# Optimization experiments

Measured on AMD Instinct MI355X. Metric: run time of the kernel, lower is better.

Reference implementation:

```python
import jax, jax.numpy as jnp
import numpy as np

B, F, V, E = 16384, 39, 100000, 16
D0, D1, D2 = 32, 32, 32

def setup_inputs() -> dict:
    key = jax.random.key(0)
    ks = jax.random.split(key, 12)
    return {
        "Xi": jax.random.randint(ks[0], (B, F, 1), 0, V),
        "Xv": jax.random.uniform(ks[1], (B, F), dtype=jnp.float32),
        "emb_tables": jax.random.normal(ks[2], (F, V, E), dtype=jnp.float32),
        "w_first": jax.random.normal(ks[3], (D0, F, E), dtype=jnp.float32),
        "w_inner": jax.random.normal(ks[4], (D0, F, E), dtype=jnp.float32),
        "lin1_W": jax.random.normal(ks[5], (D1, D0), dtype=jnp.float32) * 0.1,
        "lin1_b": jax.random.normal(ks[6], (D1,), dtype=jnp.float32) * 0.1,
        "lin2_W": jax.random.normal(ks[7], (D2, D1), dtype=jnp.float32) * 0.1,
        "lin2_b": jax.random.normal(ks[8], (D2,), dtype=jnp.float32) * 0.1,
        "last_W": jax.random.normal(ks[9], (1, D2), dtype=jnp.float32) * 0.1,
        "last_b": jax.random.normal(ks[10], (1,), dtype=jnp.float32) * 0.1,
    }

def reference(Xi, Xv, emb_tables, w_first, w_inner, lin1_W, lin1_b, lin2_W, lin2_b, last_W, last_b):
    idx = Xi[:, :, 0]                                  # [B,F]
    # per-field embedding gather, scaled by feature value
    emb = emb_tables[jnp.arange(F)[None, :], idx]      # [B,F,E]
    emb = emb * Xv[:, :, None]                         # [B,F,E]
    # first-order: nested loops over (D0, F) collapse to one einsum
    first = jnp.einsum('bfe,dfe->bd', emb, w_first)    # [B,D0]
    # inner-product second-order: (sum over fields of <emb_f, w_df>)^2
    s = jnp.einsum('bfe,dfe->bd', emb, w_inner)        # [B,D0]
    x = first + s * s
    # deep MLP (relu, no dropout/batchnorm in inference)
    x = jax.nn.relu(x @ lin1_W.T + lin1_b)
    x = jax.nn.relu(x @ lin2_W.T + lin2_b)
    x = x @ last_W.T + last_b                          # [B,1]
    return jnp.sum(x, axis=1)                          # [B]
```

## Files before the change

kernel.cpp:

```cpp
#include <hip/hip_runtime.h>


namespace {

typedef _Float16 half8 __attribute__((ext_vector_type(8)));
typedef _Float16 half4 __attribute__((ext_vector_type(4)));
typedef float floatx4 __attribute__((ext_vector_type(4)));
typedef float f32x4 __attribute__((ext_vector_type(4)));

constexpr int Bn = 16384;
constexpr int Fn = 39;
constexpr int Vn = 100000;
constexpr int En = 16;
constexpr int M = 32;
constexpr int KST = 20;
constexpr int NRT = Bn / 16;
constexpr int WBLOCKS = 20;
constexpr int AWS_OFF_H = 65536;
constexpr int GITER = 10;

__device__ __forceinline__ half8 cvt8(float4 a, float4 b) {
    half8 h;
    h[0] = (_Float16)a.x; h[1] = (_Float16)a.y;
    h[2] = (_Float16)a.z; h[3] = (_Float16)a.w;
    h[4] = (_Float16)b.x; h[5] = (_Float16)b.y;
    h[6] = (_Float16)b.z; h[7] = (_Float16)b.w;
    return h;
}

__device__ __forceinline__ half4 cvt4s(f32x4 a, float s) {
    half4 h;
    h[0] = (_Float16)(a[0] * s);
    h[1] = (_Float16)(a[1] * s);
    h[2] = (_Float16)(a[2] * s);
    h[3] = (_Float16)(a[3] * s);
    return h;
}

__global__ __launch_bounds__(256) void pnn_stage(
    const int* __restrict__ Xi,
    const float* __restrict__ Xv,
    const float* __restrict__ T,
    const float* __restrict__ w_first,
    const float* __restrict__ w_inner,
    _Float16* __restrict__ ws)
{
    _Float16* __restrict__ Wws = ws;
    _Float16* __restrict__ Aws = ws + AWS_OFF_H;

    const int tid = threadIdx.x;

    if (blockIdx.x >= NRT) {
        const int slot = (blockIdx.x - NRT) * 256 + tid;
        const int t16 = slot / (KST * 64);
        const int rem = slot % (KST * 64);
        const int t = rem >> 6;
        const int lane = rem & 63;
        const int n = t16 * 16 + (lane & 15);
        const int kb = t * 32 + (lane >> 4) * 8;
        half8 h = {0, 0, 0, 0, 0, 0, 0, 0};
        if (!(t == KST - 1 && (lane >> 4) >= 2)) {
            const float* src = ((n < 32) ? (w_first + (size_t)n * 624)
                                         : (w_inner + (size_t)(n - 32) * 624)) + kb;
            const float4 a = *reinterpret_cast<const float4*>(src);
            const float4 b = *reinterpret_cast<const float4*>(src + 4);
            h = cvt8(a, b);
        }
        *reinterpret_cast<half8*>(Wws + (size_t)slot * 8) = h;
        return;
    }

    __shared__ _Float16 At[KST * 512];
    __shared__ int   xi[624];
    __shared__ float xv[624];

    const int rt = blockIdx.x;
    const int r0 = rt * 16;

    if (tid < 156) {
        reinterpret_cast<int4*>(xi)[tid] =
            reinterpret_cast<const int4*>(Xi + (size_t)r0 * Fn)[tid];
        reinterpret_cast<float4*>(xv)[tid] =
            reinterpret_cast<const float4*>(Xv + (size_t)r0 * Fn)[tid];
    }
    if (tid < 32) {
        half8 z = {0, 0, 0, 0, 0, 0, 0, 0};
        *reinterpret_cast<half8*>(At + ((KST - 1) * 64 + 32 + tid) * 8) = z;
    }
    __syncthreads();

    f32x4 v[GITER];
    float s[GITER];
    int   slot[GITER];
    bool  ok[GITER];
#pragma unroll
    for (int it = 0; it < GITER; ++it) {
        const int i = tid + it * 256;
        ok[it] = (i < 16 * Fn * 4);
        if (ok[it]) {
            const int j = i >> 2, c = i & 3;
            const int r = j & 15, f = j >> 4;
            const int idx = xi[r * Fn + f];
            s[it] = xv[r * Fn + f];
            const f32x4* src = reinterpret_cast<const f32x4*>(
                T + ((size_t)f * Vn + (size_t)idx) * En + c * 4);
            v[it] = __builtin_nontemporal_load(src);
            slot[it] = (((f >> 1) * 64) + (f & 1) * 32 + r) * 8
                       + (c >> 1) * 128 + (c & 1) * 4;
        }
    }
#pragma unroll
    for (int it = 0; it < GITER; ++it) {
        if (ok[it])
            *reinterpret_cast<half4*>(At + slot[it]) = cvt4s(v[it], s[it]);
    }
    __syncthreads();

    const int4* s4 = reinterpret_cast<const int4*>(At);
    int4* d4 = reinterpret_cast<int4*>(Aws + (size_t)rt * KST * 512);
#pragma unroll
    for (int j = 0; j < 5; ++j) d4[tid + j * 256] = s4[tid + j * 256];
}

struct SMemE {
    float x[M * 69];
    float wsh[2176];
    float r1[1024];
    float r2[1024];
};

__global__ __launch_bounds__(512) void pnn_gemm(
    const _Float16* __restrict__ ws,
    const float* __restrict__ lin1_W,
    const float* __restrict__ lin1_b,
    const float* __restrict__ lin2_W,
    const float* __restrict__ lin2_b,
    const float* __restrict__ last_W,
    const float* __restrict__ last_b,
    float* __restrict__ out)
{
    __shared__ SMemE sm;

    const _Float16* __restrict__ Wws = ws;
    const _Float16* __restrict__ Aws = ws + AWS_OFF_H;

    const int tid = threadIdx.x;
    const int lane = tid & 63;
    const int wv = tid >> 6;
    const int q = wv & 1;
    const int t16 = wv >> 1;
    const int row0 = blockIdx.x * M;

    const _Float16* aptr = Aws + ((size_t)(blockIdx.x * 2 + q) * KST) * 512 + lane * 8;
    const _Float16* bptr = Wws + ((size_t)t16 * KST) * 512 + lane * 8;

    floatx4 acc = {0.0f, 0.0f, 0.0f, 0.0f};
#pragma unroll
    for (int t = 0; t < KST; ++t) {
        const half8 af = *reinterpret_cast<const half8*>(aptr + t * 512);
        const half8 bf = *reinterpret_cast<const half8*>(bptr + t * 512);
        acc = __builtin_amdgcn_mfma_f32_16x16x32_f16(af, bf, acc, 0, 0, 0);
    }

    {
        const int col = t16 * 16 + (lane & 15);
        const int rbase = q * 16 + (lane >> 4) * 4;
#pragma unroll
        for (int r = 0; r < 4; ++r)
            sm.x[(rbase + r) * 69 + col] = acc[r];
    }

    for (int i = tid; i < 2145; i += 512) {
        float v;
        if (i < 1024)      v = lin1_W[i];
        else if (i < 2048) v = lin2_W[i - 1024];
        else if (i < 2080) v = lin1_b[i - 2048];
        else if (i < 2112) v = lin2_b[i - 2080];
        else if (i < 2144) v = last_W[i - 2112];
        else               v = last_b[0];
        sm.wsh[i] = v;
    }
    __syncthreads();

    for (int p = tid; p < 1024; p += 512) {
        const int j = p >> 5, r = p & 31;
        const float fi = sm.x[r * 69 + j];
        const float sq = sm.x[r * 69 + 32 + j];
        sm.r1[j * 32 + r] = fi + sq * sq;
    }
    __syncthreads();

    {
        const int r = tid & 31, n0 = (tid >> 5) * 2;
        float a0 = sm.wsh[2048 + n0];
        float a1 = sm.wsh[2048 + n0 + 1];
#pragma unroll
        for (int j = 0; j < 32; ++j) {
            const float xj = sm.r1[j * 32 + r];
            a0 = fmaf(sm.wsh[n0 * 32 + j],       xj, a0);
            a1 = fmaf(sm.wsh[(n0 + 1) * 32 + j], xj, a1);
        }
        sm.r2[n0 * 32 + r]       = fmaxf(a0, 0.0f);
        sm.r2[(n0 + 1) * 32 + r] = fmaxf(a1, 0.0f);
    }
    __syncthreads();

    {
        const int r = tid & 31, n0 = (tid >> 5) * 2;
        float a0 = sm.wsh[2080 + n0];
        float a1 = sm.wsh[2080 + n0 + 1];
#pragma unroll
        for (int j = 0; j < 32; ++j) {
            const float xj = sm.r2[j * 32 + r];
            a0 = fmaf(sm.wsh[1024 + n0 * 32 + j],       xj, a0);
            a1 = fmaf(sm.wsh[1024 + (n0 + 1) * 32 + j], xj, a1);
        }
        sm.r1[n0 * 32 + r]       = fmaxf(a0, 0.0f);
        sm.r1[(n0 + 1) * 32 + r] = fmaxf(a1, 0.0f);
    }
    __syncthreads();

    if (tid < M) {
        float res = sm.wsh[2144];
#pragma unroll
        for (int j = 0; j < 32; ++j)
            res = fmaf(sm.wsh[2112 + j], sm.r1[j * 32 + tid], res);
        out[row0 + tid] = res;
    }
}

}

extern "C" void kernel_launch(void* const* d_in, const int* in_sizes, int n_in,
                              void* d_out, int out_size, void* d_ws, size_t ws_size,
                              hipStream_t stream) {
    (void)in_sizes; (void)n_in; (void)out_size; (void)ws_size;
    const int*   Xi      = (const int*)d_in[0];
    const float* Xv      = (const float*)d_in[1];
    const float* T       = (const float*)d_in[2];
    const float* w_first = (const float*)d_in[3];
    const float* w_inner = (const float*)d_in[4];
    const float* lin1_W  = (const float*)d_in[5];
    const float* lin1_b  = (const float*)d_in[6];
    const float* lin2_W  = (const float*)d_in[7];
    const float* lin2_b  = (const float*)d_in[8];
    const float* last_W  = (const float*)d_in[9];
    const float* last_b  = (const float*)d_in[10];
    float* out = (float*)d_out;
    _Float16* ws = (_Float16*)d_ws;

    hipLaunchKernelGGL(pnn_stage, dim3(NRT + WBLOCKS), dim3(256), 0, stream,
                       Xi, Xv, T, w_first, w_inner, ws);
    hipLaunchKernelGGL(pnn_gemm, dim3(Bn / M), dim3(512), 0, stream,
                       ws, lin1_W, lin1_b, lin2_W, lin2_b, last_W, last_b, out);
}
```

Baseline: 320.0 us.

## Fuse embedding gather, MFMA GEMM and MLP into a single kernel

Merges the staging kernel and the GEMM/MLP kernel into one launch. Each 512-thread block gathers and scales the embeddings for 32 rows straight into LDS as fp16, and the MFMA reads A from LDS. The weight matrix is loaded from global fp32 and converted per block instead of being pre-staged. This removes the workspace round trip and one launch, but every block now re-converts the shared weights and holds the gather and MLP buffers in the same LDS union.

```diff
diff --git a/kernel.cpp b/kernel.cpp
--- a/kernel.cpp
+++ b/kernel.cpp
@@ -14,9 +14,6 @@
 constexpr int En = 16;
 constexpr int M = 32;
 constexpr int KST = 20;
-constexpr int NRT = Bn / 16;
-constexpr int WBLOCKS = 20;
-constexpr int AWS_OFF_H = 65536;
 constexpr int GITER = 10;
 
 __device__ __forceinline__ half8 cvt8(float4 a, float4 b) {
@@ -37,100 +34,30 @@
     return h;
 }
 
-__global__ __launch_bounds__(256) void pnn_stage(
+struct SMemGather {
+    _Float16 At[2][KST * 512];
+    int   xi[M * Fn];
+    float xv[M * Fn];
+};
+
+struct SMemMlp {
+    float x[M * 69];
+    float wsh[2176];
+    float r1[1024];
+    float r2[1024];
+};
+
+union SMemU {
+    SMemGather g;
+    SMemMlp m;
+};
+
+__global__ __launch_bounds__(512, 4) void pnn_fused(
     const int* __restrict__ Xi,
     const float* __restrict__ Xv,
     const float* __restrict__ T,
     const float* __restrict__ w_first,
     const float* __restrict__ w_inner,
-    _Float16* __restrict__ ws)
-{
-    _Float16* __restrict__ Wws = ws;
-    _Float16* __restrict__ Aws = ws + AWS_OFF_H;
-
-    const int tid = threadIdx.x;
-
-    if (blockIdx.x >= NRT) {
-        const int slot = (blockIdx.x - NRT) * 256 + tid;
-        const int t16 = slot / (KST * 64);
-        const int rem = slot % (KST * 64);
-        const int t = rem >> 6;
-        const int lane = rem & 63;
-        const int n = t16 * 16 + (lane & 15);
-        const int kb = t * 32 + (lane >> 4) * 8;
-        half8 h = {0, 0, 0, 0, 0, 0, 0, 0};
-        if (!(t == KST - 1 && (lane >> 4) >= 2)) {
-            const float* src = ((n < 32) ? (w_first + (size_t)n * 624)
-                                         : (w_inner + (size_t)(n - 32) * 624)) + kb;
-            const float4 a = *reinterpret_cast<const float4*>(src);
-            const float4 b = *reinterpret_cast<const float4*>(src + 4);
-            h = cvt8(a, b);
-        }
-        *reinterpret_cast<half8*>(Wws + (size_t)slot * 8) = h;
-        return;
-    }
-
-    __shared__ _Float16 At[KST * 512];
-    __shared__ int   xi[624];
-    __shared__ float xv[624];
-
-    const int rt = blockIdx.x;
-    const int r0 = rt * 16;
-
-    if (tid < 156) {
-        reinterpret_cast<int4*>(xi)[tid] =
-            reinterpret_cast<const int4*>(Xi + (size_t)r0 * Fn)[tid];
-        reinterpret_cast<float4*>(xv)[tid] =
-            reinterpret_cast<const float4*>(Xv + (size_t)r0 * Fn)[tid];
-    }
-    if (tid < 32) {
-        half8 z = {0, 0, 0, 0, 0, 0, 0, 0};
-        *reinterpret_cast<half8*>(At + ((KST - 1) * 64 + 32 + tid) * 8) = z;
-    }
-    __syncthreads();
-
-    f32x4 v[GITER];
-    float s[GITER];
-    int   slot[GITER];
-    bool  ok[GITER];
-#pragma unroll
-    for (int it = 0; it < GITER; ++it) {
-        const int i = tid + it * 256;
-        ok[it] = (i < 16 * Fn * 4);
-        if (ok[it]) {
-            const int j = i >> 2, c = i & 3;
-            const int r = j & 15, f = j >> 4;
-            const int idx = xi[r * Fn + f];
-            s[it] = xv[r * Fn + f];
-            const f32x4* src = reinterpret_cast<const f32x4*>(
-                T + ((size_t)f * Vn + (size_t)idx) * En + c * 4);
-            v[it] = __builtin_nontemporal_load(src);
-            slot[it] = (((f >> 1) * 64) + (f & 1) * 32 + r) * 8
-                       + (c >> 1) * 128 + (c & 1) * 4;
-        }
-    }
-#pragma unroll
-    for (int it = 0; it < GITER; ++it) {
-        if (ok[it])
-            *reinterpret_cast<half4*>(At + slot[it]) = cvt4s(v[it], s[it]);
-    }
-    __syncthreads();
-
-    const int4* s4 = reinterpret_cast<const int4*>(At);
-    int4* d4 = reinterpret_cast<int4*>(Aws + (size_t)rt * KST * 512);
-#pragma unroll
-    for (int j = 0; j < 5; ++j) d4[tid + j * 256] = s4[tid + j * 256];
-}
-
-struct SMemE {
-    float x[M * 69];
-    float wsh[2176];
-    float r1[1024];
-    float r2[1024];
-};
-
-__global__ __launch_bounds__(512) void pnn_gemm(
-    const _Float16* __restrict__ ws,
     const float* __restrict__ lin1_W,
     const float* __restrict__ lin1_b,
     const float* __restrict__ lin2_W,
@@ -139,10 +66,7 @@
     const float* __restrict__ last_b,
     float* __restrict__ out)
 {
-    __shared__ SMemE sm;
-
-    const _Float16* __restrict__ Wws = ws;
-    const _Float16* __restrict__ Aws = ws + AWS_OFF_H;
+    __shared__ SMemU sm;
 
     const int tid = threadIdx.x;
     const int lane = tid & 63;
@@ -151,80 +75,136 @@
     const int t16 = wv >> 1;
     const int row0 = blockIdx.x * M;
 
-    const _Float16* aptr = Aws + ((size_t)(blockIdx.x * 2 + q) * KST) * 512 + lane * 8;
-    const _Float16* bptr = Wws + ((size_t)t16 * KST) * 512 + lane * 8;
+    if (tid < 312) {
+        reinterpret_cast<int4*>(sm.g.xi)[tid] =
+            reinterpret_cast<const int4*>(Xi + (size_t)row0 * Fn)[tid];
+        reinterpret_cast<float4*>(sm.g.xv)[tid] =
+            reinterpret_cast<const float4*>(Xv + (size_t)row0 * Fn)[tid];
+    }
+    if (tid < 64) {
+        half8 z = {0, 0, 0, 0, 0, 0, 0, 0};
+        const int qq = tid >> 5;
+        *reinterpret_cast<half8*>(
+            &sm.g.At[qq][((KST - 1) * 64 + 32 + (tid & 31)) * 8]) = z;
+    }
+    __syncthreads();
+
+    f32x4 v[GITER];
+    float s[GITER];
+    int   slot[GITER];
+    bool  ok[GITER];
+#pragma unroll
+    for (int it = 0; it < GITER; ++it) {
+        const int i = tid + it * 512;
+        ok[it] = (i < M * Fn * 4);
+        if (ok[it]) {
+            const int j = i >> 2, c = i & 3;
+            const int r = j & 31, f = j >> 5;
+            const int idx = sm.g.xi[r * Fn + f];
+            s[it] = sm.g.xv[r * Fn + f];
+            const f32x4* src = reinterpret_cast<const f32x4*>(
+                T + ((size_t)f * Vn + (size_t)idx) * En + c * 4);
+            v[it] = __builtin_nontemporal_load(src);
+            slot[it] = (r >> 4) * (KST * 512)
+                     + (((f >> 1) * 64) + (f & 1) * 32 + (r & 15)) * 8
+                     + (c >> 1) * 128 + (c & 1) * 4;
+        }
+    }
+#pragma unroll
+    for (int it = 0; it < GITER; ++it) {
+        if (ok[it])
+            *reinterpret_cast<half4*>(&sm.g.At[0][0] + slot[it]) =
+                cvt4s(v[it], s[it]);
+    }
+    __syncthreads();
+
+    const int n = t16 * 16 + (lane & 15);
+    const int kq = lane >> 4;
+    const float* wrow = (n < 32) ? (w_first + (size_t)n * 624)
+                                 : (w_inner + (size_t)(n - 32) * 624);
+    const _Float16* aLds = &sm.g.At[q][lane * 8];
 
     floatx4 acc = {0.0f, 0.0f, 0.0f, 0.0f};
 #pragma unroll
     for (int t = 0; t < KST; ++t) {
-        const half8 af = *reinterpret_cast<const half8*>(aptr + t * 512);
-        const half8 bf = *reinterpret_cast<const half8*>(bptr + t * 512);
+        const half8 af = *reinterpret_cast<const half8*>(aLds + t * 512);
+        half8 bf;
+        if (t == KST - 1 && kq >= 2) {
+            bf = half8{0, 0, 0, 0, 0, 0, 0, 0};
+        } else {
+            const int kb = t * 32 + kq * 8;
+            const float4 a = *reinterpret_cast<const float4*>(wrow + kb);
+            const float4 b = *reinterpret_cast<const float4*>(wrow + kb + 4);
+            bf = cvt8(a, b);
+        }
         acc = __builtin_amdgcn_mfma_f32_16x16x32_f16(af, bf, acc, 0, 0, 0);
     }
+
+    __syncthreads();
 
     {
         const int col = t16 * 16 + (lane & 15);
         const int rbase = q * 16 + (lane >> 4) * 4;
 #pragma unroll
         for (int r = 0; r < 4; ++r)
-            sm.x[(rbase + r) * 69 + col] = acc[r];
+            sm.m.x[(rbase + r) * 69 + col] = acc[r];
     }
 
     for (int i = tid; i < 2145; i += 512) {
-        float v;
-        if (i < 1024)      v = lin1_W[i];
-        else if (i < 2048) v = lin2_W[i - 1024];
-        else if (i < 2080) v = lin1_b[i - 2048];
-        else if (i < 2112) v = lin2_b[i - 2080];
-        else if (i < 2144) v = last_W[i - 2112];
-        else               v = last_b[0];
-        sm.wsh[i] = v;
+        float vv;
+        if (i < 1024)      vv = lin1_W[i];
+        else if (i < 2048) vv = lin2_W[i - 1024];
+        else if (i < 2080) vv = lin1_b[i - 2048];
+        else if (i < 2112) vv = lin2_b[i - 2080];
+        else if (i < 2144) vv = last_W[i - 2112];
+        else               vv = last_b[0];
+        sm.m.wsh[i] = vv;
     }
     __syncthreads();
 
     for (int p = tid; p < 1024; p += 512) {
         const int j = p >> 5, r = p & 31;
-        const float fi = sm.x[r * 69 + j];
-        const float sq = sm.x[r * 69 + 32 + j];
-        sm.r1[j * 32 + r] = fi + sq * sq;
+        const float fi = sm.m.x[r * 69 + j];
+        const float sq = sm.m.x[r * 69 + 32 + j];
+        sm.m.r1[j * 32 + r] = fi + sq * sq;
     }
     __syncthreads();
 
     {
         const int r = tid & 31, n0 = (tid >> 5) * 2;
-        float a0 = sm.wsh[2048 + n0];
-        float a1 = sm.wsh[2048 + n0 + 1];
+        float a0 = sm.m.wsh[2048 + n0];
+        float a1 = sm.m.wsh[2048 + n0 + 1];
 #pragma unroll
         for (int j = 0; j < 32; ++j) {
-            const float xj = sm.r1[j * 32 + r];
-            a0 = fmaf(sm.wsh[n0 * 32 + j],       xj, a0);
-            a1 = fmaf(sm.wsh[(n0 + 1) * 32 + j], xj, a1);
-        }
-        sm.r2[n0 * 32 + r]       = fmaxf(a0, 0.0f);
-        sm.r2[(n0 + 1) * 32 + r] = fmaxf(a1, 0.0f);
+            const float xj = sm.m.r1[j * 32 + r];
+            a0 = fmaf(sm.m.wsh[n0 * 32 + j],       xj, a0);
+            a1 = fmaf(sm.m.wsh[(n0 + 1) * 32 + j], xj, a1);
+        }
+        sm.m.r2[n0 * 32 + r]       = fmaxf(a0, 0.0f);
+        sm.m.r2[(n0 + 1) * 32 + r] = fmaxf(a1, 0.0f);
     }
     __syncthreads();
 
     {
         const int r = tid & 31, n0 = (tid >> 5) * 2;
-        float a0 = sm.wsh[2080 + n0];
-        float a1 = sm.wsh[2080 + n0 + 1];
+        float a0 = sm.m.wsh[2080 + n0];
+        float a1 = sm.m.wsh[2080 + n0 + 1];
 #pragma unroll
         for (int j = 0; j < 32; ++j) {
-            const float xj = sm.r2[j * 32 + r];
-            a0 = fmaf(sm.wsh[1024 + n0 * 32 + j],       xj, a0);
-            a1 = fmaf(sm.wsh[1024 + (n0 + 1) * 32 + j], xj, a1);
-        }
-        sm.r1[n0 * 32 + r]       = fmaxf(a0, 0.0f);
-        sm.r1[(n0 + 1) * 32 + r] = fmaxf(a1, 0.0f);
+            const float xj = sm.m.r2[j * 32 + r];
+            a0 = fmaf(sm.m.wsh[1024 + n0 * 32 + j],       xj, a0);
+            a1 = fmaf(sm.m.wsh[1024 + (n0 + 1) * 32 + j], xj, a1);
+        }
+        sm.m.r1[n0 * 32 + r]       = fmaxf(a0, 0.0f);
+        sm.m.r1[(n0 + 1) * 32 + r] = fmaxf(a1, 0.0f);
     }
     __syncthreads();
 
     if (tid < M) {
-        float res = sm.wsh[2144];
+        float res = sm.m.wsh[2144];
 #pragma unroll
         for (int j = 0; j < 32; ++j)
-            res = fmaf(sm.wsh[2112 + j], sm.r1[j * 32 + tid], res);
+            res = fmaf(sm.m.wsh[2112 + j], sm.m.r1[j * 32 + tid], res);
         out[row0 + tid] = res;
     }
 }
@@ -234,7 +214,7 @@
 extern "C" void kernel_launch(void* const* d_in, const int* in_sizes, int n_in,
                               void* d_out, int out_size, void* d_ws, size_t ws_size,
                               hipStream_t stream) {
-    (void)in_sizes; (void)n_in; (void)out_size; (void)ws_size;
+    (void)in_sizes; (void)n_in; (void)out_size; (void)d_ws; (void)ws_size;
     const int*   Xi      = (const int*)d_in[0];
     const float* Xv      = (const float*)d_in[1];
     const float* T       = (const float*)d_in[2];
@@ -247,10 +227,8 @@
     const float* last_W  = (const float*)d_in[9];
     const float* last_b  = (const float*)d_in[10];
     float* out = (float*)d_out;
-    _Float16* ws = (_Float16*)d_ws;
-
-    hipLaunchKernelGGL(pnn_stage, dim3(NRT + WBLOCKS), dim3(256), 0, stream,
-                       Xi, Xv, T, w_first, w_inner, ws);
-    hipLaunchKernelGGL(pnn_gemm, dim3(Bn / M), dim3(512), 0, stream,
-                       ws, lin1_W, lin1_b, lin2_W, lin2_b, last_W, last_b, out);
-}
+
+    hipLaunchKernelGGL(pnn_fused, dim3(Bn / M), dim3(512), 0, stream,
+                       Xi, Xv, T, w_first, w_inner,
+                       lin1_W, lin1_b, lin2_W, lin2_b, last_W, last_b, out);
+}
```

After: 319.1 us (median of 2 runs). Within noise of the previous version (-0.3%).
